# Performance work log

Measured on AMD Instinct MI355X. Metric: run time of the kernel, lower is better.

The kernel has to match this reference:

```python
import jax, jax.numpy as jnp
import numpy as np

NEG = -9.0e15
BN_EPS = 1e-5


def _build_graph():
    N = 22
    A = np.eye(N, dtype=np.float32)
    for i in range(N - 1):
        A[i, i + 1] = 1.0
        A[i + 1, i] = 1.0
    distal = [3, 7, 11, 15, 16, 20, 21]
    jl = [0, 1, 2, 3, 17, 18, 19, 20, 21]
    jr = [4, 5, 6, 7, 12, 13, 14, 15, 16]
    adj_sym = np.zeros((N, N), dtype=np.float32)
    for i in range(N):
        adj_sym[i, i] = 1.0
        if i in jl:
            adj_sym[i, jr[jl.index(i)]] = 1.0
        if i in jr:
            adj_sym[i, jl[jr.index(i)]] = 1.0
    A1 = A.copy()
    for i in distal:
        A1[i] = 0.0
    A2 = np.linalg.matrix_power(A, 2)
    A3 = np.linalg.matrix_power(A, 3)
    for i in range(N):
        if i not in distal:
            A2[i] = 0.0
            A3[i] = 0.0
    adj_con = A1 + A2 + A3
    return adj_sym, adj_con


def setup_inputs() -> dict:
    key = jax.random.key(0)
    B, T, N, C, O = 64, 50, 22, 64, 64
    adj_sym, adj_con = _build_graph()
    rs, cs = np.nonzero(adj_sym > 0)  # row-major, matches torch nonzero order
    rc, cc = np.nonzero(adj_con > 0)
    ks = jax.random.split(key, 11)
    f32 = jnp.float32
    return {
        "x": jax.random.normal(ks[0], (B, T, N, C), f32),
        "W_sym": 0.1 * jax.random.normal(ks[1], (2, C, O), f32),
        "e_sym": 1.0 + 0.1 * jax.random.normal(ks[2], (O, len(rs)), f32),
        "W_con": 0.1 * jax.random.normal(ks[3], (2, C, O), f32),
        "e_con": 1.0 + 0.1 * jax.random.normal(ks[4], (O, len(rc)), f32),
        "W_dis": 0.1 * jax.random.normal(ks[5], (C, O), f32),
        "att": 0.1 * jax.random.normal(ks[6], (N, N), f32),
        "b_dis": 0.1 * jax.random.normal(ks[7], (O,), f32),
        "cat_w": 0.05 * jax.random.normal(ks[8], (O, 3 * O), f32),
        "gammas": 1.0 + 0.1 * jax.random.normal(ks[9], (4, O), f32),
        "betas": 0.1 * jax.random.normal(ks[10], (4, O), f32),
        "rows_sym": jnp.asarray(rs, jnp.int32),
        "cols_sym": jnp.asarray(cs, jnp.int32),
        "rows_con": jnp.asarray(rc, jnp.int32),
        "cols_con": jnp.asarray(cc, jnp.int32),
    }


def _semch(x, W, e, rows, cols):
    # x: [B,T,N,C], W: [2,C,O], e: [O,nnz] -> [B,T,N,O]
    N = x.shape[2]
    O = W.shape[2]
    h0 = x @ W[0]  # [B,T,N,O]
    h1 = x @ W[1]
    logits = jnp.full((O, N, N), NEG, x.dtype).at[:, rows, cols].set(e)
    A = jax.nn.softmax(logits, axis=2)  # per-channel masked softmax over rows
    diag = A[:, jnp.arange(N), jnp.arange(N)]  # [O,N]
    A_off = A * (1.0 - jnp.eye(N, dtype=x.dtype))
    return h0 * diag.T[None, None] + jnp.einsum('cij,btjc->btic', A_off, h1)


def _bn_relu(h, g, b):
    # training-mode BatchNorm2d over [B,C,T,N], stats on (0,2,3)
    mu = h.mean(axis=(0, 2, 3), keepdims=True)
    var = ((h - mu) ** 2).mean(axis=(0, 2, 3), keepdims=True)
    out = (h - mu) * jax.lax.rsqrt(var + BN_EPS) * g[None, :, None, None] + b[None, :, None, None]
    return jax.nn.relu(out)


def reference(x, W_sym, e_sym, W_con, e_con, W_dis, att, b_dis, cat_w,
              gammas, betas, rows_sym, cols_sym, rows_con, cols_con):
    xs = _semch(x, W_sym, e_sym, rows_sym, cols_sym)  # [B,T,N,O]
    yc = _semch(x, W_con, e_con, rows_con, cols_con)  # [B,T,N,O]
    # pairwise distance branch: pos_rel [B,T,N,N,C], summed over dim 2
    pos_rel = x[:, :, :, None, :] - x[:, :, None, :, :]
    dis = jnp.sqrt(jnp.sum(pos_rel * pos_rel, axis=2)) + 1e-8  # [B,T,N,C]
    z = jnp.einsum('ij,btjo->btio', att, dis @ W_dis) + b_dis  # GraphConvolution
    # to NCHW: [B,O,T,N]
    xp = _bn_relu(xs.transpose(0, 3, 1, 2), gammas[0], betas[0])
    yp = _bn_relu(yc.transpose(0, 3, 1, 2), gammas[1], betas[1])
    zp = _bn_relu(z.transpose(0, 3, 1, 2), gammas[2], betas[2])
    cat = jnp.concatenate((xp, yp, zp), axis=1)  # [B,3O,T,N]
    out = jnp.einsum('of,bftn->botn', cat_w, cat)  # 1x1 conv
    out = _bn_relu(out, gammas[3], betas[3])
    return out.transpose(0, 2, 3, 1)  # [B,T,N,O]
```

## Files before the change

### kernel.cpp

```cpp
#include <hip/hip_runtime.h>
#include <hip/hip_bf16.h>

typedef __hip_bfloat16 bf16;
typedef __attribute__((ext_vector_type(8))) short bf16x8;
typedef __attribute__((ext_vector_type(4))) float f32x4;

#define BT     3200
#define N_     22
#define NO     1408
#define NN     484
#define BTN    70400
#define ELEMS  4505600
#define MAXNZ  128
#define NSHARD 16
#define STATSZ (NSHARD * 384 + 8 * 128)

static __device__ __forceinline__ bf16  f2bf(float v) { return __float2bfloat16(v); }
static __device__ __forceinline__ short fbf(float v) {
    bf16 h = __float2bfloat16(v);
    return *reinterpret_cast<short*>(&h);
}
static __device__ __forceinline__ float sbf(short s) {
    return __uint_as_float(((unsigned)(unsigned short)s) << 16);
}
static __device__ __forceinline__ void unp(unsigned u, float& lo, float& hi) {
    lo = __uint_as_float(u << 16);
    hi = __uint_as_float(u & 0xffff0000u);
}

__global__ void prep_kernel(const float* __restrict__ e_s, const int* __restrict__ rs,
                            const int* __restrict__ cs, int nnz_s,
                            const float* __restrict__ e_c, const int* __restrict__ rc,
                            const int* __restrict__ cc, int nnz_c,
                            const float* __restrict__ cat_w,
                            const float* __restrict__ Wsym, const float* __restrict__ Wcon,
                            const float* __restrict__ Wdis, const float* __restrict__ att,
                            short* __restrict__ AAb, short* __restrict__ CB,
                            short* __restrict__ WB, int* __restrict__ ej,
                            short* __restrict__ attF, float* __restrict__ stats) {
    const int tid = threadIdx.x;
    if (blockIdx.x < 2) {
        __shared__ float eL[64 * (MAXNZ + 1)];
        __shared__ int rowsL[MAXNZ], colsL[MAXNZ];
        const int t = blockIdx.x;
        const float* e    = t ? e_c : e_s;
        const int*   rows = t ? rc  : rs;
        const int*   cols = t ? cc  : cs;
        const int    nnz  = t ? nnz_c : nnz_s;
        const int    str  = nnz + 1;

        for (int idx = tid; idx < 64 * nnz; idx += 256) {
            int o = idx / nnz, k = idx - o * nnz;
            eL[o * str + k] = expf(e[idx]);
        }
        for (int idx = tid; idx < nnz; idx += 256) { rowsL[idx] = rows[idx]; colsL[idx] = cols[idx]; }
        __syncthreads();

        const int o = tid & 63, ig = tid >> 6;
        float s[6];
        #pragma unroll
        for (int q = 0; q < 6; q++) s[q] = 0.f;
        for (int k = 0; k < nnz; k++) {
            int r = rowsL[k];
            float ev = eL[o * str + k];
            #pragma unroll
            for (int q = 0; q < 6; q++)
                if (r == ig + 4 * q) s[q] += ev;
        }
        float inv[6];
        #pragma unroll
        for (int q = 0; q < 6; q++) inv[q] = 1.f / s[q];
        for (int k = 0; k < nnz; k++) {
            int r = rowsL[k];
            #pragma unroll
            for (int q = 0; q < 6; q++)
                if (r == ig + 4 * q)
                    AAb[((size_t)(r * N_ + colsL[k]) * 64 + o) * 2 + t] =
                        fbf(eL[o * str + k] * inv[q]);
        }
    } else if (blockIdx.x < 8) {
        int gi = (blockIdx.x - 2) * 256 + tid;
        if (gi >= 1536) return;
        int nt = gi / 384, rem = gi % 384;
        int kc = rem >> 6, L = rem & 63;
        int n = nt * 16 + (L & 15);
        int kbase = kc * 32 + (L >> 4) * 8;
        float4 w0 = *(const float4*)&cat_w[n * 192 + kbase];
        float4 w1 = *(const float4*)&cat_w[n * 192 + kbase + 4];
        bf16x8 frag;
        frag[0] = fbf(w0.x); frag[1] = fbf(w0.y); frag[2] = fbf(w0.z); frag[3] = fbf(w0.w);
        frag[4] = fbf(w1.x); frag[5] = fbf(w1.y); frag[6] = fbf(w1.z); frag[7] = fbf(w1.w);
        ((bf16x8*)CB)[gi] = frag;
    } else if (blockIdx.x < 18) {
        int gi = (blockIdx.x - 8) * 256 + tid;
        if (gi >= 2560) return;
        int L = gi & 63;
        int q = gi >> 6;
        int nt = q & 3;
        int pk = q >> 2;
        int kc = pk & 1;
        int p  = pk >> 1;
        const float* Wsrc = (p == 0) ? Wsym :
                            (p == 1) ? Wsym + 4096 :
                            (p == 2) ? Wcon :
                            (p == 3) ? Wcon + 4096 : Wdis;
        int n  = nt * 16 + (L & 15);
        int kb = kc * 32 + (L >> 4) * 8;
        bf16x8 frag;
        #pragma unroll
        for (int j = 0; j < 8; j++) frag[j] = fbf(Wsrc[(kb + j) * 64 + n]);
        ((bf16x8*)WB)[gi] = frag;
    } else {
        for (int idx = tid; idx < STATSZ; idx += 256) stats[idx] = 0.f;
        if (tid < N_) {
            unsigned bits = 0u;
            for (int e = 0; e < nnz_s; e++)
                if (rs[e] == tid && cs[e] != tid) bits |= 1u << cs[e];
            for (int e = 0; e < nnz_c; e++)
                if (rc[e] == tid && cc[e] != tid) bits |= 1u << cc[e];
            int cnt = 0;
            unsigned b = bits;
            while (b) { int j = __ffs(b) - 1; b &= b - 1; ej[tid * 8 + cnt++] = j; }
            int js = 0;
            while (((bits >> js) & 1u) || js == tid) js++;
            for (; cnt < 8; cnt++) ej[tid * 8 + cnt] = js;
        }
        for (int f = tid; f < 128; f += 256) {
            int rt = f >> 6, LL = f & 63;
            int row = rt * 16 + (LL & 15);
            int kb  = (LL >> 4) * 8;
            bf16x8 frag;
            #pragma unroll
            for (int j = 0; j < 8; j++) {
                int k = kb + j;
                float vv = (row < N_ && k < N_) ? att[row * N_ + k] : 0.f;
                frag[j] = fbf(vv);
            }
            ((bf16x8*)attF)[f] = frag;
        }
    }
}

__launch_bounds__(256)
__global__ void fused_hmix(const float* __restrict__ x, const short* __restrict__ WB,
                           const short* __restrict__ AAb, const short* __restrict__ attF,
                           const int* __restrict__ ej, const float* __restrict__ bdis,
                           bf16* __restrict__ xs, bf16* __restrict__ yc,
                           bf16* __restrict__ z, float* __restrict__ stats1) {
    __shared__ __align__(16) char smem[14784];
    short*    xl   = (short*)smem;
    short*    dl   = (short*)(smem + 4096);
    float*    red4 = (float*)(smem + 8192);
    unsigned* pp0  = (unsigned*)smem;
    unsigned* pp1  = (unsigned*)(smem + 5632);
    short*    p2   = (short*)(smem + 11264);
    int*      ejL  = (int*)(smem + 14080);
    float*    red  = (float*)smem;

    const int g   = blockIdx.x;
    const int tid = threadIdx.x;
    const size_t base = (size_t)g * NO;
    const int w = tid >> 6, L = tid & 63;
    const int lane16 = L & 15, quad = L >> 4;
    const int colw = w * 16 + lane16;
    const bf16x8* WBf = (const bf16x8*)WB;

    if (tid < 176) ejL[tid] = ej[tid];
    float v[6], s = 0.f, s2 = 0.f;
    #pragma unroll
    for (int k = 0; k < 6; k++) {
        int i = w + 4 * k;
        float t = (i < N_) ? x[base + i * 64 + L] : 0.f;
        v[k] = t; s += t; s2 += t * t;
    }
    red4[w * 64 + L]       = s;
    red4[256 + w * 64 + L] = s2;
    for (int idx = tid; idx < 320; idx += 256) {
        ((unsigned*)xl)[704 + idx] = 0u;
        ((unsigned*)dl)[704 + idx] = 0u;
    }
    __syncthreads();
    float S  = (red4[L] + red4[64 + L]) + (red4[128 + L] + red4[192 + L]);
    float S2 = (red4[256 + L] + red4[320 + L]) + (red4[384 + L] + red4[448 + L]);
    #pragma unroll
    for (int k = 0; k < 6; k++) {
        int i = w + 4 * k;
        if (i < N_) {
            float t = v[k];
            float d2 = S2 - 2.f * t * S + (float)N_ * t * t;
            float d  = sqrtf(fmaxf(d2, 0.f)) + 1e-8f;
            int ci = i * 64 + (L ^ ((i & 7) << 3));
            xl[ci] = fbf(t);
            dl[ci] = fbf(d);
        }
    }
    __syncthreads();

    f32x4 acc[5][2];
    #pragma unroll
    for (int p = 0; p < 5; p++)
        #pragma unroll
        for (int rt = 0; rt < 2; rt++) acc[p][rt] = (f32x4){0.f, 0.f, 0.f, 0.f};

    #pragma unroll
    for (int kc = 0; kc < 2; kc++) {
        bf16x8 ax[2], ad[2];
        #pragma unroll
        for (int rt = 0; rt < 2; rt++) {
            int row = rt * 16 + lane16;
            int ci  = row * 64 + ((kc * 32 + quad * 8) ^ ((row & 7) << 3));
            ax[rt] = *(const bf16x8*)(xl + ci);
            ad[rt] = *(const bf16x8*)(dl + ci);
        }
        #pragma unroll
        for (int p = 0; p < 5; p++) {
            bf16x8 bw = WBf[((p * 2 + kc) * 4 + w) * 64 + L];
            #pragma unroll
            for (int rt = 0; rt < 2; rt++) {
                bf16x8 a = (p < 4) ? ax[rt] : ad[rt];
                acc[p][rt] = __builtin_amdgcn_mfma_f32_16x16x32_bf16(a, bw, acc[p][rt], 0, 0, 0);
            }
        }
    }
    __syncthreads();

    #pragma unroll
    for (int rt = 0; rt < 2; rt++)
        #pragma unroll
        for (int r = 0; r < 4; r++) {
            int m = rt * 16 + quad * 4 + r;
            if (m < N_) {
                float h0s = acc[0][rt][r], h1s = acc[1][rt][r];
                float h0c = acc[2][rt][r], h1c = acc[3][rt][r];
                pp0[m * 64 + colw] = (unsigned)(unsigned short)fbf(h1s) |
                                     ((unsigned)(unsigned short)fbf(h0s) << 16);
                pp1[m * 64 + colw] = (unsigned)(unsigned short)fbf(h1c) |
                                     ((unsigned)(unsigned short)fbf(h0c) << 16);
                p2[m * 64 + colw] = fbf(acc[4][rt][r]);
            }
        }
    __syncthreads();

    f32x4 zacc[2];
    zacc[0] = (f32x4){0.f, 0.f, 0.f, 0.f};
    zacc[1] = (f32x4){0.f, 0.f, 0.f, 0.f};
    {
        bf16x8 bfrag;
        #pragma unroll
        for (int j = 0; j < 8; j++) {
            int k = quad * 8 + j;
            bfrag[j] = (k < N_) ? p2[k * 64 + colw] : (short)0;
        }
        const bf16x8* attFf = (const bf16x8*)attF;
        #pragma unroll
        for (int rt = 0; rt < 2; rt++)
            zacc[rt] = __builtin_amdgcn_mfma_f32_16x16x32_bf16(attFf[rt * 64 + L], bfrag,
                                                               zacc[rt], 0, 0, 0);
    }

    float mxs[6], myc[6];
    #pragma unroll
    for (int k = 0; k < 6; k++) { mxs[k] = 0.f; myc[k] = 0.f; }
    const unsigned* AAu = (const unsigned*)AAb;
    #pragma unroll
    for (int k = 0; k < 6; k++) {
        int i = w + 4 * k;
        if (i < N_) {
            #pragma unroll
            for (int e = 0; e < 8; e++) {
                int j = ejL[i * 8 + e];
                unsigned a = AAu[(size_t)(i * N_ + j) * 64 + L];
                float as, ac; unp(a, as, ac);
                mxs[k] = fmaf(as, sbf((short)pp0[j * 64 + L]), mxs[k]);
                myc[k] = fmaf(ac, sbf((short)pp1[j * 64 + L]), myc[k]);
            }
        }
    }

    float st0 = 0.f, st1 = 0.f, st2 = 0.f, st3 = 0.f;
    #pragma unroll
    for (int k = 0; k < 6; k++) {
        int i = w + 4 * k;
        if (i < N_) {
            unsigned ad2 = AAu[(size_t)(i * 23) * 64 + L];
            float asd, acd; unp(ad2, asd, acd);
            float h0sv = __uint_as_float(pp0[i * 64 + L] & 0xffff0000u);
            float h0cv = __uint_as_float(pp1[i * 64 + L] & 0xffff0000u);
            float xsv = mxs[k] + asd * h0sv;
            float ycv = myc[k] + acd * h0cv;
            size_t oi = base + i * 64 + L;
            xs[oi] = f2bf(xsv); yc[oi] = f2bf(ycv);
            st0 += xsv; st1 += xsv * xsv;
            st2 += ycv; st3 += ycv * ycv;
        }
    }

    float bd = bdis[colw];
    float st4 = 0.f, st5 = 0.f;
    #pragma unroll
    for (int rt = 0; rt < 2; rt++)
        #pragma unroll
        for (int r = 0; r < 4; r++) {
            int m = rt * 16 + quad * 4 + r;
            if (m < N_) {
                float zv = zacc[rt][r] + bd;
                z[base + (size_t)m * 64 + colw] = f2bf(zv);
                st4 += zv; st5 += zv * zv;
            }
        }
    st4 += __shfl_xor(st4, 16); st4 += __shfl_xor(st4, 32);
    st5 += __shfl_xor(st5, 16); st5 += __shfl_xor(st5, 32);

    __syncthreads();
    red[(w * 4 + 0) * 64 + L] = st0;
    red[(w * 4 + 1) * 64 + L] = st1;
    red[(w * 4 + 2) * 64 + L] = st2;
    red[(w * 4 + 3) * 64 + L] = st3;
    if (quad == 0) { red[16 * 64 + colw] = st4; red[17 * 64 + colw] = st5; }
    __syncthreads();
    float* myStats = stats1 + (size_t)(g & (NSHARD - 1)) * 384;
    for (int qq = tid; qq < 384; qq += 256) {
        int q = qq >> 6, o = qq & 63;
        float vv;
        if (q < 4)
            vv = (red[q * 64 + o] + red[(4 + q) * 64 + o]) +
                 (red[(8 + q) * 64 + o] + red[(12 + q) * 64 + o]);
        else
            vv = red[(12 + q) * 64 + o];
        atomicAdd(&myStats[qq], vv);
    }
}

__launch_bounds__(256)
__global__ void mix_pass(const bf16* __restrict__ xs, const bf16* __restrict__ yc,
                         const bf16* __restrict__ z, const float* __restrict__ stats1,
                         const float* __restrict__ gammas, const float* __restrict__ betas,
                         const short* __restrict__ CB,
                         bf16* __restrict__ out2, float* __restrict__ stats2) {
    __shared__ float sL[384];
    __shared__ float red[512];

    const int tid = threadIdx.x;
    const int w = tid >> 6, L = tid & 63;
    const int lane16 = L & 15, quad = L >> 4;
    const int R0 = blockIdx.x * 64 + w * 16;

    if (tid < 192) {
        int t = tid >> 6, o = tid & 63;
        float S = 0.f, SS = 0.f;
        for (int s = 0; s < NSHARD; s++) {
            S  += stats1[s * 384 + (2 * t) * 64 + o];
            SS += stats1[s * 384 + (2 * t + 1) * 64 + o];
        }
        const float invn = 1.f / (float)BTN;
        float mu   = S * invn;
        float var  = SS * invn - mu * mu;
        float rstd = rsqrtf(var + 1e-5f);
        float a = gammas[t * 64 + o] * rstd;
        float c = betas[t * 64 + o] - mu * a;
        sL[t * 128 + o]      = a;
        sL[t * 128 + 64 + o] = c;
    }
    __syncthreads();

    const bf16* srcs[3] = { xs, yc, z };

    f32x4 acc[4];
    #pragma unroll
    for (int nt = 0; nt < 4; nt++) acc[nt] = (f32x4){0.f, 0.f, 0.f, 0.f};

    #pragma unroll
    for (int kc = 0; kc < 6; kc++) {
        const int src = kc >> 1;
        const int c0  = (kc & 1) * 32 + quad * 8;
        int row = R0 + lane16;
        uint4 u = *(const uint4*)(srcs[src] + (size_t)row * 64 + c0);
        float v[8];
        unp(u.x, v[0], v[1]); unp(u.y, v[2], v[3]);
        unp(u.z, v[4], v[5]); unp(u.w, v[6], v[7]);
        bf16x8 av;
        #pragma unroll
        for (int e = 0; e < 8; e++) {
            float t = fmaxf(fmaf(v[e], sL[src * 128 + c0 + e],
                                 sL[src * 128 + 64 + c0 + e]), 0.f);
            av[e] = fbf(t);
        }
        #pragma unroll
        for (int nt = 0; nt < 4; nt++) {
            bf16x8 bw = ((const bf16x8*)CB)[(nt * 6 + kc) * 64 + L];
            acc[nt] = __builtin_amdgcn_mfma_f32_16x16x32_bf16(av, bw, acc[nt], 0, 0, 0);
        }
    }

    float s[4]  = {0.f, 0.f, 0.f, 0.f};
    float s2[4] = {0.f, 0.f, 0.f, 0.f};
    #pragma unroll
    for (int nt = 0; nt < 4; nt++)
        #pragma unroll
        for (int r = 0; r < 4; r++) {
            int row = R0 + quad * 4 + r;
            int col = nt * 16 + lane16;
            float v = acc[nt][r];
            out2[(size_t)row * 64 + col] = f2bf(v);
            s[nt] += v; s2[nt] += v * v;
        }
    #pragma unroll
    for (int nt = 0; nt < 4; nt++) {
        s[nt]  += __shfl_xor(s[nt], 16);
        s[nt]  += __shfl_xor(s[nt], 32);
        s2[nt] += __shfl_xor(s2[nt], 16);
        s2[nt] += __shfl_xor(s2[nt], 32);
    }
    if (quad == 0) {
        #pragma unroll
        for (int nt = 0; nt < 4; nt++) {
            red[w * 64 + nt * 16 + lane16]       = s[nt];
            red[256 + w * 64 + nt * 16 + lane16] = s2[nt];
        }
    }
    __syncthreads();
    float* myStats = stats2 + (size_t)(blockIdx.x & 7) * 128;
    if (tid < 64) {
        float t = red[tid] + red[64 + tid] + red[128 + tid] + red[192 + tid];
        atomicAdd(&myStats[tid], t);
    } else if (tid < 128) {
        int c = tid - 64;
        float t = red[256 + c] + red[320 + c] + red[384 + c] + red[448 + c];
        atomicAdd(&myStats[64 + c], t);
    }
}

__launch_bounds__(256)
__global__ void final_pass(const bf16* __restrict__ out2, const float* __restrict__ stats2,
                           const float* __restrict__ gammas, const float* __restrict__ betas,
                           float* __restrict__ out) {
    __shared__ float sc[128];
    const int tid = threadIdx.x;
    if (tid < 64) {
        int o = tid;
        float S = 0.f, SS = 0.f;
        for (int s = 0; s < 8; s++) {
            S  += stats2[s * 128 + o];
            SS += stats2[s * 128 + 64 + o];
        }
        const float invn = 1.f / (float)BTN;
        float mu   = S * invn;
        float var  = SS * invn - mu * mu;
        float rstd = rsqrtf(var + 1e-5f);
        float a = gammas[192 + o] * rstd;
        float c = betas[192 + o] - mu * a;
        sc[o]      = a;
        sc[64 + o] = c;
    }
    __syncthreads();
    #pragma unroll
    for (int j = 0; j < 4; j++) {
        int gid = blockIdx.x * 1024 + j * 256 + tid;
        ushort4 u = reinterpret_cast<const ushort4*>(out2)[gid];
        const int o = (gid * 4) & 63;
        float f0, f1, f2, f3;
        unp((unsigned)u.x | ((unsigned)u.y << 16), f0, f1);
        unp((unsigned)u.z | ((unsigned)u.w << 16), f2, f3);
        float4 r;
        r.x = fmaxf(fmaf(f0, sc[o],     sc[64 + o]),     0.f);
        r.y = fmaxf(fmaf(f1, sc[o + 1], sc[64 + o + 1]), 0.f);
        r.z = fmaxf(fmaf(f2, sc[o + 2], sc[64 + o + 2]), 0.f);
        r.w = fmaxf(fmaf(f3, sc[o + 3], sc[64 + o + 3]), 0.f);
        reinterpret_cast<float4*>(out)[gid] = r;
    }
}

extern "C" void kernel_launch(void* const* d_in, const int* in_sizes, int n_in,
                              void* d_out, int out_size, void* d_ws, size_t ws_size,
                              hipStream_t stream) {
    const float* x      = (const float*)d_in[0];
    const float* W_sym  = (const float*)d_in[1];
    const float* e_sym  = (const float*)d_in[2];
    const float* W_con  = (const float*)d_in[3];
    const float* e_con  = (const float*)d_in[4];
    const float* W_dis  = (const float*)d_in[5];
    const float* att    = (const float*)d_in[6];
    const float* b_dis  = (const float*)d_in[7];
    const float* cat_w  = (const float*)d_in[8];
    const float* gammas = (const float*)d_in[9];
    const float* betas  = (const float*)d_in[10];
    const int* rows_sym = (const int*)d_in[11];
    const int* cols_sym = (const int*)d_in[12];
    const int* rows_con = (const int*)d_in[13];
    const int* cols_con = (const int*)d_in[14];
    const int nnz_s = in_sizes[2] / 64;
    const int nnz_c = in_sizes[4] / 64;

    char* p = (char*)d_ws;
    float* stats  = (float*)p; p += (size_t)STATSZ * 4;
    short* AAb    = (short*)p; p += (size_t)NN * 64 * 2 * 2;
    short* CB     = (short*)p; p += (size_t)1536 * 8 * 2;
    short* WB     = (short*)p; p += (size_t)2560 * 8 * 2;
    int*   ej     = (int*)p;   p += 192 * 4;
    short* attF   = (short*)p; p += 128 * 16;
    bf16*  xsb    = (bf16*)p;  p += (size_t)ELEMS * 2;
    bf16*  ycb    = (bf16*)p;  p += (size_t)ELEMS * 2;
    bf16*  zb     = (bf16*)p;  p += (size_t)ELEMS * 2;
    bf16*  out2   = (bf16*)p;  p += (size_t)ELEMS * 2;
    float* stats1 = stats;
    float* stats2 = stats + NSHARD * 384;

    hipMemsetAsync(AAb, 0, (size_t)NN * 64 * 2 * 2, stream);
    prep_kernel<<<19, 256, 0, stream>>>(e_sym, rows_sym, cols_sym, nnz_s,
                                        e_con, rows_con, cols_con, nnz_c,
                                        cat_w, W_sym, W_con, W_dis, att,
                                        AAb, CB, WB, ej, attF, stats);
    fused_hmix<<<BT, 256, 0, stream>>>(x, WB, AAb, attF, ej, b_dis,
                                       xsb, ycb, zb, stats1);
    mix_pass<<<1100, 256, 0, stream>>>(xsb, ycb, zb, stats1, gammas, betas,
                                       CB, out2, stats2);
    final_pass<<<1100, 256, 0, stream>>>(out2, stats2, gammas, betas, (float*)d_out);
}
```

Before: 172.6 us.

## Process two time slices per hmix block with x prefetch and packed neighbor indices

fused_hmix now handles two (b,t) slices per block and launches half as many blocks. The second slice's x values are loaded into registers while the first slice's LDS staging happens, so the global load latency can overlap compute. The neighbor index table becomes one packed 64-bit word per node, held in registers instead of an LDS copy, and the zero-fill of the padded LDS rows is removed. This amortizes per-block setup (weights, bias, index loads, stat atomics) over more work, at the cost of fewer blocks for latency hiding and more synchronisations per block.

```diff
diff --git a/kernel.cpp b/kernel.cpp
--- a/kernel.cpp
+++ b/kernel.cpp
@@ -36,7 +36,7 @@
                             const float* __restrict__ Wsym, const float* __restrict__ Wcon,
                             const float* __restrict__ Wdis, const float* __restrict__ att,
                             short* __restrict__ AAb, short* __restrict__ CB,
-                            short* __restrict__ WB, int* __restrict__ ej,
+                            short* __restrict__ WB, unsigned long long* __restrict__ ej64,
                             short* __restrict__ attF, float* __restrict__ stats) {
     const int tid = threadIdx.x;
     if (blockIdx.x < 2) {
@@ -118,12 +118,17 @@
                 if (rs[e] == tid && cs[e] != tid) bits |= 1u << cs[e];
             for (int e = 0; e < nnz_c; e++)
                 if (rc[e] == tid && cc[e] != tid) bits |= 1u << cc[e];
+            unsigned long long pack = 0ull;
             int cnt = 0;
             unsigned b = bits;
-            while (b) { int j = __ffs(b) - 1; b &= b - 1; ej[tid * 8 + cnt++] = j; }
+            while (b) {
+                int j = __ffs(b) - 1; b &= b - 1;
+                pack |= (unsigned long long)j << (8 * cnt); cnt++;
+            }
             int js = 0;
             while (((bits >> js) & 1u) || js == tid) js++;
-            for (; cnt < 8; cnt++) ej[tid * 8 + cnt] = js;
+            for (; cnt < 8; cnt++) pack |= (unsigned long long)js << (8 * cnt);
+            ej64[tid] = pack;
         }
         for (int f = tid; f < 128; f += 256) {
             int rt = f >> 6, LL = f & 63;
@@ -144,174 +149,193 @@
 __launch_bounds__(256)
 __global__ void fused_hmix(const float* __restrict__ x, const short* __restrict__ WB,
                            const short* __restrict__ AAb, const short* __restrict__ attF,
-                           const int* __restrict__ ej, const float* __restrict__ bdis,
+                           const unsigned long long* __restrict__ ej64,
+                           const float* __restrict__ bdis,
                            bf16* __restrict__ xs, bf16* __restrict__ yc,
                            bf16* __restrict__ z, float* __restrict__ stats1) {
-    __shared__ __align__(16) char smem[14784];
+    __shared__ __align__(16) char smem[14080];
     short*    xl   = (short*)smem;
     short*    dl   = (short*)(smem + 4096);
     float*    red4 = (float*)(smem + 8192);
     unsigned* pp0  = (unsigned*)smem;
     unsigned* pp1  = (unsigned*)(smem + 5632);
     short*    p2   = (short*)(smem + 11264);
-    int*      ejL  = (int*)(smem + 14080);
     float*    red  = (float*)smem;
 
     const int g   = blockIdx.x;
     const int tid = threadIdx.x;
-    const size_t base = (size_t)g * NO;
+    const size_t base0 = (size_t)g * 2 * NO;
     const int w = tid >> 6, L = tid & 63;
     const int lane16 = L & 15, quad = L >> 4;
     const int colw = w * 16 + lane16;
     const bf16x8* WBf = (const bf16x8*)WB;
-
-    if (tid < 176) ejL[tid] = ej[tid];
-    float v[6], s = 0.f, s2 = 0.f;
+    const unsigned* AAu = (const unsigned*)AAb;
+
+    unsigned long long e8[6];
     #pragma unroll
     for (int k = 0; k < 6; k++) {
         int i = w + 4 * k;
-        float t = (i < N_) ? x[base + i * 64 + L] : 0.f;
-        v[k] = t; s += t; s2 += t * t;
-    }
-    red4[w * 64 + L]       = s;
-    red4[256 + w * 64 + L] = s2;
-    for (int idx = tid; idx < 320; idx += 256) {
-        ((unsigned*)xl)[704 + idx] = 0u;
-        ((unsigned*)dl)[704 + idx] = 0u;
-    }
-    __syncthreads();
-    float S  = (red4[L] + red4[64 + L]) + (red4[128 + L] + red4[192 + L]);
-    float S2 = (red4[256 + L] + red4[320 + L]) + (red4[384 + L] + red4[448 + L]);
+        e8[k] = (i < N_) ? ej64[i] : 0ull;
+    }
+    const float bd = bdis[colw];
+
+    float st0 = 0.f, st1 = 0.f, st2 = 0.f, st3 = 0.f, st4 = 0.f, st5 = 0.f;
+
+    float v[6];
     #pragma unroll
     for (int k = 0; k < 6; k++) {
         int i = w + 4 * k;
-        if (i < N_) {
-            float t = v[k];
-            float d2 = S2 - 2.f * t * S + (float)N_ * t * t;
-            float d  = sqrtf(fmaxf(d2, 0.f)) + 1e-8f;
-            int ci = i * 64 + (L ^ ((i & 7) << 3));
-            xl[ci] = fbf(t);
-            dl[ci] = fbf(d);
-        }
-    }
-    __syncthreads();
-
-    f32x4 acc[5][2];
-    #pragma unroll
-    for (int p = 0; p < 5; p++)
-        #pragma unroll
-        for (int rt = 0; rt < 2; rt++) acc[p][rt] = (f32x4){0.f, 0.f, 0.f, 0.f};
-
-    #pragma unroll
-    for (int kc = 0; kc < 2; kc++) {
-        bf16x8 ax[2], ad[2];
-        #pragma unroll
-        for (int rt = 0; rt < 2; rt++) {
-            int row = rt * 16 + lane16;
-            int ci  = row * 64 + ((kc * 32 + quad * 8) ^ ((row & 7) << 3));
-            ax[rt] = *(const bf16x8*)(xl + ci);
-            ad[rt] = *(const bf16x8*)(dl + ci);
-        }
-        #pragma unroll
-        for (int p = 0; p < 5; p++) {
-            bf16x8 bw = WBf[((p * 2 + kc) * 4 + w) * 64 + L];
+        v[k] = (i < N_) ? x[base0 + i * 64 + L] : 0.f;
+    }
+
+    #pragma unroll
+    for (int bt = 0; bt < 2; ++bt) {
+        const size_t base = base0 + (size_t)bt * NO;
+
+        float s = 0.f, s2 = 0.f;
+        #pragma unroll
+        for (int k = 0; k < 6; k++) { s += v[k]; s2 += v[k] * v[k]; }
+        red4[w * 64 + L]       = s;
+        red4[256 + w * 64 + L] = s2;
+        __syncthreads();
+        float S  = (red4[L] + red4[64 + L]) + (red4[128 + L] + red4[192 + L]);
+        float S2 = (red4[256 + L] + red4[320 + L]) + (red4[384 + L] + red4[448 + L]);
+        #pragma unroll
+        for (int k = 0; k < 6; k++) {
+            int i = w + 4 * k;
+            if (i < N_) {
+                float t = v[k];
+                float d2 = S2 - 2.f * t * S + (float)N_ * t * t;
+                float d  = sqrtf(fmaxf(d2, 0.f)) + 1e-8f;
+                int ci = i * 64 + (L ^ ((i & 7) << 3));
+                xl[ci] = fbf(t);
+                dl[ci] = fbf(d);
+            }
+        }
+        if (bt == 0) {
+            #pragma unroll
+            for (int k = 0; k < 6; k++) {
+                int i = w + 4 * k;
+                v[k] = (i < N_) ? x[base0 + NO + i * 64 + L] : 0.f;
+            }
+        }
+        __syncthreads();
+
+        f32x4 acc[5][2];
+        #pragma unroll
+        for (int p = 0; p < 5; p++)
+            #pragma unroll
+            for (int rt = 0; rt < 2; rt++) acc[p][rt] = (f32x4){0.f, 0.f, 0.f, 0.f};
+
+        #pragma unroll
+        for (int kc = 0; kc < 2; kc++) {
+            bf16x8 ax[2], ad[2];
             #pragma unroll
             for (int rt = 0; rt < 2; rt++) {
-                bf16x8 a = (p < 4) ? ax[rt] : ad[rt];
-                acc[p][rt] = __builtin_amdgcn_mfma_f32_16x16x32_bf16(a, bw, acc[p][rt], 0, 0, 0);
-            }
-        }
-    }
-    __syncthreads();
-
-    #pragma unroll
-    for (int rt = 0; rt < 2; rt++)
-        #pragma unroll
-        for (int r = 0; r < 4; r++) {
-            int m = rt * 16 + quad * 4 + r;
-            if (m < N_) {
-                float h0s = acc[0][rt][r], h1s = acc[1][rt][r];
-                float h0c = acc[2][rt][r], h1c = acc[3][rt][r];
-                pp0[m * 64 + colw] = (unsigned)(unsigned short)fbf(h1s) |
-                                     ((unsigned)(unsigned short)fbf(h0s) << 16);
-                pp1[m * 64 + colw] = (unsigned)(unsigned short)fbf(h1c) |
-                                     ((unsigned)(unsigned short)fbf(h0c) << 16);
-                p2[m * 64 + colw] = fbf(acc[4][rt][r]);
-            }
-        }
-    __syncthreads();
-
-    f32x4 zacc[2];
-    zacc[0] = (f32x4){0.f, 0.f, 0.f, 0.f};
-    zacc[1] = (f32x4){0.f, 0.f, 0.f, 0.f};
-    {
-        bf16x8 bfrag;
-        #pragma unroll
-        for (int j = 0; j < 8; j++) {
-            int k = quad * 8 + j;
-            bfrag[j] = (k < N_) ? p2[k * 64 + colw] : (short)0;
-        }
-        const bf16x8* attFf = (const bf16x8*)attF;
+                int row = rt * 16 + lane16;
+                int ci  = row * 64 + ((kc * 32 + quad * 8) ^ ((row & 7) << 3));
+                ax[rt] = *(const bf16x8*)(xl + ci);
+                ad[rt] = *(const bf16x8*)(dl + ci);
+            }
+            #pragma unroll
+            for (int p = 0; p < 5; p++) {
+                bf16x8 bw = WBf[((p * 2 + kc) * 4 + w) * 64 + L];
+                #pragma unroll
+                for (int rt = 0; rt < 2; rt++) {
+                    bf16x8 a = (p < 4) ? ax[rt] : ad[rt];
+                    acc[p][rt] = __builtin_amdgcn_mfma_f32_16x16x32_bf16(a, bw, acc[p][rt], 0, 0, 0);
+                }
+            }
+        }
+        __syncthreads();
+
         #pragma unroll
         for (int rt = 0; rt < 2; rt++)
-            zacc[rt] = __builtin_amdgcn_mfma_f32_16x16x32_bf16(attFf[rt * 64 + L], bfrag,
-                                                               zacc[rt], 0, 0, 0);
-    }
-
-    float mxs[6], myc[6];
-    #pragma unroll
-    for (int k = 0; k < 6; k++) { mxs[k] = 0.f; myc[k] = 0.f; }
-    const unsigned* AAu = (const unsigned*)AAb;
-    #pragma unroll
-    for (int k = 0; k < 6; k++) {
-        int i = w + 4 * k;
-        if (i < N_) {
-            #pragma unroll
-            for (int e = 0; e < 8; e++) {
-                int j = ejL[i * 8 + e];
-                unsigned a = AAu[(size_t)(i * N_ + j) * 64 + L];
-                float as, ac; unp(a, as, ac);
-                mxs[k] = fmaf(as, sbf((short)pp0[j * 64 + L]), mxs[k]);
-                myc[k] = fmaf(ac, sbf((short)pp1[j * 64 + L]), myc[k]);
-            }
-        }
-    }
-
-    float st0 = 0.f, st1 = 0.f, st2 = 0.f, st3 = 0.f;
-    #pragma unroll
-    for (int k = 0; k < 6; k++) {
-        int i = w + 4 * k;
-        if (i < N_) {
-            unsigned ad2 = AAu[(size_t)(i * 23) * 64 + L];
-            float asd, acd; unp(ad2, asd, acd);
-            float h0sv = __uint_as_float(pp0[i * 64 + L] & 0xffff0000u);
-            float h0cv = __uint_as_float(pp1[i * 64 + L] & 0xffff0000u);
-            float xsv = mxs[k] + asd * h0sv;
-            float ycv = myc[k] + acd * h0cv;
-            size_t oi = base + i * 64 + L;
-            xs[oi] = f2bf(xsv); yc[oi] = f2bf(ycv);
-            st0 += xsv; st1 += xsv * xsv;
-            st2 += ycv; st3 += ycv * ycv;
-        }
-    }
-
-    float bd = bdis[colw];
-    float st4 = 0.f, st5 = 0.f;
-    #pragma unroll
-    for (int rt = 0; rt < 2; rt++)
-        #pragma unroll
-        for (int r = 0; r < 4; r++) {
-            int m = rt * 16 + quad * 4 + r;
-            if (m < N_) {
-                float zv = zacc[rt][r] + bd;
-                z[base + (size_t)m * 64 + colw] = f2bf(zv);
-                st4 += zv; st5 += zv * zv;
-            }
-        }
+            #pragma unroll
+            for (int r = 0; r < 4; r++) {
+                int m = rt * 16 + quad * 4 + r;
+                if (m < N_) {
+                    float h0s = acc[0][rt][r], h1s = acc[1][rt][r];
+                    float h0c = acc[2][rt][r], h1c = acc[3][rt][r];
+                    pp0[m * 64 + colw] = (unsigned)(unsigned short)fbf(h1s) |
+                                         ((unsigned)(unsigned short)fbf(h0s) << 16);
+                    pp1[m * 64 + colw] = (unsigned)(unsigned short)fbf(h1c) |
+                                         ((unsigned)(unsigned short)fbf(h0c) << 16);
+                    p2[m * 64 + colw] = fbf(acc[4][rt][r]);
+                }
+            }
+        __syncthreads();
+
+        f32x4 zacc[2];
+        zacc[0] = (f32x4){0.f, 0.f, 0.f, 0.f};
+        zacc[1] = (f32x4){0.f, 0.f, 0.f, 0.f};
+        {
+            bf16x8 bfrag;
+            #pragma unroll
+            for (int j = 0; j < 8; j++) {
+                int k = quad * 8 + j;
+                bfrag[j] = (k < N_) ? p2[k * 64 + colw] : (short)0;
+            }
+            const bf16x8* attFf = (const bf16x8*)attF;
+            #pragma unroll
+            for (int rt = 0; rt < 2; rt++)
+                zacc[rt] = __builtin_amdgcn_mfma_f32_16x16x32_bf16(attFf[rt * 64 + L], bfrag,
+                                                                   zacc[rt], 0, 0, 0);
+        }
+
+        float mxs[6], myc[6];
+        #pragma unroll
+        for (int k = 0; k < 6; k++) { mxs[k] = 0.f; myc[k] = 0.f; }
+        #pragma unroll
+        for (int k = 0; k < 6; k++) {
+            int i = w + 4 * k;
+            if (i < N_) {
+                #pragma unroll
+                for (int e = 0; e < 8; e++) {
+                    int j = (int)((e8[k] >> (8 * e)) & 0xff);
+                    unsigned a = AAu[(size_t)(i * N_ + j) * 64 + L];
+                    float as, ac; unp(a, as, ac);
+                    mxs[k] = fmaf(as, sbf((short)pp0[j * 64 + L]), mxs[k]);
+                    myc[k] = fmaf(ac, sbf((short)pp1[j * 64 + L]), myc[k]);
+                }
+            }
+        }
+
+        #pragma unroll
+        for (int k = 0; k < 6; k++) {
+            int i = w + 4 * k;
+            if (i < N_) {
+                unsigned ad2 = AAu[(size_t)(i * 23) * 64 + L];
+                float asd, acd; unp(ad2, asd, acd);
+                float h0sv = __uint_as_float(pp0[i * 64 + L] & 0xffff0000u);
+                float h0cv = __uint_as_float(pp1[i * 64 + L] & 0xffff0000u);
+                float xsv = mxs[k] + asd * h0sv;
+                float ycv = myc[k] + acd * h0cv;
+                size_t oi = base + i * 64 + L;
+                xs[oi] = f2bf(xsv); yc[oi] = f2bf(ycv);
+                st0 += xsv; st1 += xsv * xsv;
+                st2 += ycv; st3 += ycv * ycv;
+            }
+        }
+
+        #pragma unroll
+        for (int rt = 0; rt < 2; rt++)
+            #pragma unroll
+            for (int r = 0; r < 4; r++) {
+                int m = rt * 16 + quad * 4 + r;
+                if (m < N_) {
+                    float zv = zacc[rt][r] + bd;
+                    z[base + (size_t)m * 64 + colw] = f2bf(zv);
+                    st4 += zv; st5 += zv * zv;
+                }
+            }
+
+        __syncthreads();
+    }
+
     st4 += __shfl_xor(st4, 16); st4 += __shfl_xor(st4, 32);
     st5 += __shfl_xor(st5, 16); st5 += __shfl_xor(st5, 32);
 
-    __syncthreads();
     red[(w * 4 + 0) * 64 + L] = st0;
     red[(w * 4 + 1) * 64 + L] = st1;
     red[(w * 4 + 2) * 64 + L] = st2;
@@ -496,7 +520,7 @@
     short* AAb    = (short*)p; p += (size_t)NN * 64 * 2 * 2;
     short* CB     = (short*)p; p += (size_t)1536 * 8 * 2;
     short* WB     = (short*)p; p += (size_t)2560 * 8 * 2;
-    int*   ej     = (int*)p;   p += 192 * 4;
+    unsigned long long* ej64 = (unsigned long long*)p; p += 24 * 8;
     short* attF   = (short*)p; p += 128 * 16;
     bf16*  xsb    = (bf16*)p;  p += (size_t)ELEMS * 2;
     bf16*  ycb    = (bf16*)p;  p += (size_t)ELEMS * 2;
@@ -509,9 +533,9 @@
     prep_kernel<<<19, 256, 0, stream>>>(e_sym, rows_sym, cols_sym, nnz_s,
                                         e_con, rows_con, cols_con, nnz_c,
                                         cat_w, W_sym, W_con, W_dis, att,
-                                        AAb, CB, WB, ej, attF, stats);
-    fused_hmix<<<BT, 256, 0, stream>>>(x, WB, AAb, attF, ej, b_dis,
-                                       xsb, ycb, zb, stats1);
+                                        AAb, CB, WB, ej64, attF, stats);
+    fused_hmix<<<BT / 2, 256, 0, stream>>>(x, WB, AAb, attF, ej64, b_dis,
+                                           xsb, ycb, zb, stats1);
     mix_pass<<<1100, 256, 0, stream>>>(xsb, ycb, zb, stats1, gammas, betas,
                                        CB, out2, stats2);
     final_pass<<<1100, 256, 0, stream>>>(out2, stats2, gammas, betas, (float*)d_out);
```

After: 185.2 us. +7.3%, slower.

## Replace padded per-row neighbor gather with compact edge list and LDS atomics

Applied to the files above, without the earlier changes.

The graph-mixing step in fused_hmix used a fixed list of 8 neighbor slots per row, padded with dummy entries. It now walks a compact global edge list of at most 96 entries split across the four waves. Each edge scatters into fp32 LDS accumulators with atomicAdd, and those accumulators are seeded with the diagonal term straight after the MFMA stage. The aim is to cut the dummy padded work and drop the bf16 packing of h1, and the separate hipMemsetAsync of AAb moves into prep_kernel. The cost is about 10 KB more shared memory per block, which may lower occupancy, plus LDS atomic contention on rows with many edges.

```diff
diff --git a/kernel.cpp b/kernel.cpp
--- a/kernel.cpp
+++ b/kernel.cpp
@@ -13,15 +13,13 @@
 #define ELEMS  4505600
 #define MAXNZ  128
 #define NSHARD 16
+#define EPAD   96
 #define STATSZ (NSHARD * 384 + 8 * 128)
 
 static __device__ __forceinline__ bf16  f2bf(float v) { return __float2bfloat16(v); }
 static __device__ __forceinline__ short fbf(float v) {
     bf16 h = __float2bfloat16(v);
     return *reinterpret_cast<short*>(&h);
-}
-static __device__ __forceinline__ float sbf(short s) {
-    return __uint_as_float(((unsigned)(unsigned short)s) << 16);
 }
 static __device__ __forceinline__ void unp(unsigned u, float& lo, float& hi) {
     lo = __uint_as_float(u << 16);
@@ -36,7 +34,7 @@
                             const float* __restrict__ Wsym, const float* __restrict__ Wcon,
                             const float* __restrict__ Wdis, const float* __restrict__ att,
                             short* __restrict__ AAb, short* __restrict__ CB,
-                            short* __restrict__ WB, int* __restrict__ ej,
+                            short* __restrict__ WB, unsigned short* __restrict__ elist,
                             short* __restrict__ attF, float* __restrict__ stats) {
     const int tid = threadIdx.x;
     if (blockIdx.x < 2) {
@@ -48,6 +46,8 @@
         const int*   cols = t ? cc  : cs;
         const int    nnz  = t ? nnz_c : nnz_s;
         const int    str  = nnz + 1;
+
+        for (int idx = tid; idx < NN * 64; idx += 256) AAb[(size_t)idx * 2 + t] = 0;
 
         for (int idx = tid; idx < 64 * nnz; idx += 256) {
             int o = idx / nnz, k = idx - o * nnz;
@@ -111,6 +111,8 @@
         for (int j = 0; j < 8; j++) frag[j] = fbf(Wsrc[(kb + j) * 64 + n]);
         ((bf16x8*)WB)[gi] = frag;
     } else {
+        __shared__ unsigned bitsL[32];
+        __shared__ int offL[32];
         for (int idx = tid; idx < STATSZ; idx += 256) stats[idx] = 0.f;
         if (tid < N_) {
             unsigned bits = 0u;
@@ -118,13 +120,27 @@
                 if (rs[e] == tid && cs[e] != tid) bits |= 1u << cs[e];
             for (int e = 0; e < nnz_c; e++)
                 if (rc[e] == tid && cc[e] != tid) bits |= 1u << cc[e];
-            int cnt = 0;
-            unsigned b = bits;
-            while (b) { int j = __ffs(b) - 1; b &= b - 1; ej[tid * 8 + cnt++] = j; }
-            int js = 0;
-            while (((bits >> js) & 1u) || js == tid) js++;
-            for (; cnt < 8; cnt++) ej[tid * 8 + cnt] = js;
-        }
+            bitsL[tid] = bits;
+        }
+        __syncthreads();
+        if (tid == 0) {
+            int off = 0;
+            for (int i = 0; i < N_; i++) { offL[i] = off; off += __popc(bitsL[i]); }
+            offL[N_] = off;
+        }
+        __syncthreads();
+        if (tid < N_) {
+            unsigned b = bitsL[tid];
+            int o = offL[tid];
+            while (b) {
+                int j = __ffs(b) - 1; b &= b - 1;
+                if (o < EPAD) elist[o] = (unsigned short)((tid << 5) | j);
+                o++;
+            }
+        }
+        int E = offL[N_] < EPAD ? offL[N_] : EPAD;
+        for (int idx = E + tid; idx < EPAD; idx += 256)
+            elist[idx] = (unsigned short)21;
         for (int f = tid; f < 128; f += 256) {
             int rt = f >> 6, LL = f & 63;
             int row = rt * 16 + (LL & 15);
@@ -144,17 +160,19 @@
 __launch_bounds__(256)
 __global__ void fused_hmix(const float* __restrict__ x, const short* __restrict__ WB,
                            const short* __restrict__ AAb, const short* __restrict__ attF,
-                           const int* __restrict__ ej, const float* __restrict__ bdis,
+                           const unsigned short* __restrict__ elist,
+                           const float* __restrict__ bdis,
                            bf16* __restrict__ xs, bf16* __restrict__ yc,
                            bf16* __restrict__ z, float* __restrict__ stats1) {
-    __shared__ __align__(16) char smem[14784];
+    __shared__ __align__(16) char smem[25536];
     short*    xl   = (short*)smem;
     short*    dl   = (short*)(smem + 4096);
     float*    red4 = (float*)(smem + 8192);
-    unsigned* pp0  = (unsigned*)smem;
-    unsigned* pp1  = (unsigned*)(smem + 5632);
+    float*    h12  = (float*)smem;
     short*    p2   = (short*)(smem + 11264);
-    int*      ejL  = (int*)(smem + 14080);
+    float*    xacc = (float*)(smem + 14080);
+    float*    yacc = (float*)(smem + 19712);
+    unsigned short* eL = (unsigned short*)(smem + 25344);
     float*    red  = (float*)smem;
 
     const int g   = blockIdx.x;
@@ -164,8 +182,9 @@
     const int lane16 = L & 15, quad = L >> 4;
     const int colw = w * 16 + lane16;
     const bf16x8* WBf = (const bf16x8*)WB;
-
-    if (tid < 176) ejL[tid] = ej[tid];
+    const unsigned* AAu = (const unsigned*)AAb;
+
+    if (tid < EPAD) eL[tid] = elist[tid];
     float v[6], s = 0.f, s2 = 0.f;
     #pragma unroll
     for (int k = 0; k < 6; k++) {
@@ -224,19 +243,26 @@
     }
     __syncthreads();
 
+    unsigned adm[8];
+    #pragma unroll
+    for (int rt = 0; rt < 2; rt++)
+        #pragma unroll
+        for (int r = 0; r < 4; r++) {
+            int m = rt * 16 + quad * 4 + r;
+            adm[rt * 4 + r] = (m < N_) ? AAu[(size_t)(m * 23) * 64 + colw] : 0u;
+        }
     #pragma unroll
     for (int rt = 0; rt < 2; rt++)
         #pragma unroll
         for (int r = 0; r < 4; r++) {
             int m = rt * 16 + quad * 4 + r;
             if (m < N_) {
-                float h0s = acc[0][rt][r], h1s = acc[1][rt][r];
-                float h0c = acc[2][rt][r], h1c = acc[3][rt][r];
-                pp0[m * 64 + colw] = (unsigned)(unsigned short)fbf(h1s) |
-                                     ((unsigned)(unsigned short)fbf(h0s) << 16);
-                pp1[m * 64 + colw] = (unsigned)(unsigned short)fbf(h1c) |
-                                     ((unsigned)(unsigned short)fbf(h0c) << 16);
-                p2[m * 64 + colw] = fbf(acc[4][rt][r]);
+                int ci = m * 64 + colw;
+                *(float2*)&h12[ci * 2] = make_float2(acc[1][rt][r], acc[3][rt][r]);
+                p2[ci] = fbf(acc[4][rt][r]);
+                float asd, acd; unp(adm[rt * 4 + r], asd, acd);
+                xacc[ci] = asd * acc[0][rt][r];
+                yacc[ci] = acd * acc[2][rt][r];
             }
         }
     __syncthreads();
@@ -258,36 +284,25 @@
                                                                zacc[rt], 0, 0, 0);
     }
 
-    float mxs[6], myc[6];
-    #pragma unroll
-    for (int k = 0; k < 6; k++) { mxs[k] = 0.f; myc[k] = 0.f; }
-    const unsigned* AAu = (const unsigned*)AAb;
+    #pragma unroll
+    for (int t = 0; t < EPAD / 4; t++) {
+        int ent = eL[t * 4 + w];
+        int i = ent >> 5, j = ent & 31;
+        unsigned a = AAu[(size_t)(i * N_ + j) * 64 + L];
+        float2 h = *(const float2*)&h12[(j * 64 + L) * 2];
+        float as, ac; unp(a, as, ac);
+        atomicAdd(&xacc[i * 64 + L], as * h.x);
+        atomicAdd(&yacc[i * 64 + L], ac * h.y);
+    }
+    __syncthreads();
+
+    float st0 = 0.f, st1 = 0.f, st2 = 0.f, st3 = 0.f;
     #pragma unroll
     for (int k = 0; k < 6; k++) {
         int i = w + 4 * k;
         if (i < N_) {
-            #pragma unroll
-            for (int e = 0; e < 8; e++) {
-                int j = ejL[i * 8 + e];
-                unsigned a = AAu[(size_t)(i * N_ + j) * 64 + L];
-                float as, ac; unp(a, as, ac);
-                mxs[k] = fmaf(as, sbf((short)pp0[j * 64 + L]), mxs[k]);
-                myc[k] = fmaf(ac, sbf((short)pp1[j * 64 + L]), myc[k]);
-            }
-        }
-    }
-
-    float st0 = 0.f, st1 = 0.f, st2 = 0.f, st3 = 0.f;
-    #pragma unroll
-    for (int k = 0; k < 6; k++) {
-        int i = w + 4 * k;
-        if (i < N_) {
-            unsigned ad2 = AAu[(size_t)(i * 23) * 64 + L];
-            float asd, acd; unp(ad2, asd, acd);
-            float h0sv = __uint_as_float(pp0[i * 64 + L] & 0xffff0000u);
-            float h0cv = __uint_as_float(pp1[i * 64 + L] & 0xffff0000u);
-            float xsv = mxs[k] + asd * h0sv;
-            float ycv = myc[k] + acd * h0cv;
+            float xsv = xacc[i * 64 + L];
+            float ycv = yacc[i * 64 + L];
             size_t oi = base + i * 64 + L;
             xs[oi] = f2bf(xsv); yc[oi] = f2bf(ycv);
             st0 += xsv; st1 += xsv * xsv;
@@ -496,7 +511,7 @@
     short* AAb    = (short*)p; p += (size_t)NN * 64 * 2 * 2;
     short* CB     = (short*)p; p += (size_t)1536 * 8 * 2;
     short* WB     = (short*)p; p += (size_t)2560 * 8 * 2;
-    int*   ej     = (int*)p;   p += 192 * 4;
+    unsigned short* elist = (unsigned short*)p; p += 256;
     short* attF   = (short*)p; p += 128 * 16;
     bf16*  xsb    = (bf16*)p;  p += (size_t)ELEMS * 2;
     bf16*  ycb    = (bf16*)p;  p += (size_t)ELEMS * 2;
@@ -505,12 +520,11 @@
     float* stats1 = stats;
     float* stats2 = stats + NSHARD * 384;
 
-    hipMemsetAsync(AAb, 0, (size_t)NN * 64 * 2 * 2, stream);
     prep_kernel<<<19, 256, 0, stream>>>(e_sym, rows_sym, cols_sym, nnz_s,
                                         e_con, rows_con, cols_con, nnz_c,
                                         cat_w, W_sym, W_con, W_dis, att,
-                                        AAb, CB, WB, ej, attF, stats);
-    fused_hmix<<<BT, 256, 0, stream>>>(x, WB, AAb, attF, ej, b_dis,
+                                        AAb, CB, WB, elist, attF, stats);
+    fused_hmix<<<BT, 256, 0, stream>>>(x, WB, AAb, attF, elist, b_dis,
                                        xsb, ycb, zb, stats1);
     mix_pass<<<1100, 256, 0, stream>>>(xsb, ycb, zb, stats1, gammas, betas,
                                        CB, out2, stats2);
```

After: 356.3 us. +106.4%, slower.
